# Kernel optimization log

Measured on AMD Instinct MI355X. Metric: run time of the kernel, lower is better.

The kernel has to match this reference:

```python
import jax, jax.numpy as jnp
import numpy as np

HID = 512
HEADS = 8
PF = 2048
EPS = 1e-5


def _layernorm(x, g, b):
    mu = jnp.mean(x, axis=-1, keepdims=True)
    var = jnp.var(x, axis=-1, keepdims=True)
    return (x - mu) * jax.lax.rsqrt(var + EPS) * g + b


def setup_inputs() -> dict:
    key = jax.random.key(0)
    ks = jax.random.split(key, 20)
    s = 0.02
    inp = {
        "trg": jax.random.normal(ks[0], (16, 1024, HID), jnp.float32),
        "src": jax.random.normal(ks[1], (16, 1024, HID), jnp.float32),
        "ln_g": jnp.ones((HID,), jnp.float32),
        "ln_b": jnp.zeros((HID,), jnp.float32),
        "wq": jax.random.normal(ks[2], (HID, HID), jnp.float32) * s,
        "bq": jnp.zeros((HID,), jnp.float32),
        "wk": jax.random.normal(ks[3], (HID, HID), jnp.float32) * s,
        "bk": jnp.zeros((HID,), jnp.float32),
        "wv": jax.random.normal(ks[4], (HID, HID), jnp.float32) * s,
        "bv": jnp.zeros((HID,), jnp.float32),
        "wo": jax.random.normal(ks[5], (HID, HID), jnp.float32) * s,
        "bo": jnp.zeros((HID,), jnp.float32),
        "pf1_w": jax.random.normal(ks[6], (PF, HID), jnp.float32) * s,
        "pf1_b": jnp.zeros((PF,), jnp.float32),
        "pf2_w": jax.random.normal(ks[7], (HID, PF), jnp.float32) * s,
        "pf2_b": jnp.zeros((HID,), jnp.float32),
        "fc1_w": jax.random.normal(ks[8], (256, HID), jnp.float32) * s,
        "fc1_b": jnp.zeros((256,), jnp.float32),
        "fc2_w": jax.random.normal(ks[9], (2, 256), jnp.float32) * s,
        "fc2_b": jnp.zeros((2,), jnp.float32),
    }
    return inp


def reference(trg, src, ln_g, ln_b, wq, bq, wk, bk, wv, bv, wo, bo,
              pf1_w, pf1_b, pf2_w, pf2_b, fc1_w, fc1_b, fc2_w, fc2_b):
    B, T, D = trg.shape
    S = src.shape[1]
    dh = D // HEADS

    # --- multi-head attention (Q=trg, K=V=src, no mask; dropout=eval/no-op) ---
    q = (trg @ wq.T + bq).reshape(B, T, HEADS, dh)
    k = (src @ wk.T + bk).reshape(B, S, HEADS, dh)
    v = (src @ wv.T + bv).reshape(B, S, HEADS, dh)
    scores = jnp.einsum('bqhd,bkhd->bhqk', q, k) / jnp.sqrt(jnp.float32(dh))
    attn = jax.nn.softmax(scores, axis=-1)
    ctx = jnp.einsum('bhqk,bkhd->bqhd', attn, v).reshape(B, T, D)
    sa_out = ctx @ wo.T + bo

    x = _layernorm(trg + sa_out, ln_g, ln_b)

    # --- position-wise feed-forward ---
    h = jax.nn.relu(x @ pf1_w.T + pf1_b)
    ff = h @ pf2_w.T + pf2_b
    x = _layernorm(x + ff, ln_g, ln_b)

    # --- norm-weighted sum pooling over sequence (vectorized) ---
    norm = jnp.linalg.norm(x, axis=2)              # [B, T]
    w = jax.nn.softmax(norm, axis=1)               # [B, T]
    pooled = jnp.einsum('bt,btd->bd', w, x)        # [B, D]

    label = jax.nn.relu(pooled @ fc1_w.T + fc1_b) @ fc2_w.T + fc2_b
    return label
```

## Files before the change

kernel.cpp:

```cpp
#include <hip/hip_runtime.h>

typedef __bf16 bf16x8 __attribute__((ext_vector_type(8)));
typedef float f32x4 __attribute__((ext_vector_type(4)));
typedef unsigned short u16;

__device__ __forceinline__ u16 f2bf(float f){
  unsigned u = __builtin_bit_cast(unsigned, f);
  u += 0x7fffu + ((u>>16)&1u);
  return (u16)(u>>16);
}
__device__ __forceinline__ float bf2f(u16 h){
  unsigned u = ((unsigned)h)<<16; return __builtin_bit_cast(float,u);
}
__device__ __forceinline__ bf16x8 ld8(const u16* p){ return *(const bf16x8*)p; }
__device__ __forceinline__ f32x4 mfma16(bf16x8 a, bf16x8 b, f32x4 c){
  return __builtin_amdgcn_mfma_f32_16x16x32_bf16(a,b,c,0,0,0);
}
__device__ __forceinline__ void gl16(const u16* g, u16* l){
  __builtin_amdgcn_global_load_lds(
    (const __attribute__((address_space(1))) unsigned int*)g,
    (__attribute__((address_space(3))) unsigned int*)l, 16, 0, 0);
}
__device__ __forceinline__ unsigned cvtpk(float a, float b){
  unsigned r;
  asm("v_cvt_pk_bf16_f32 %0, %1, %2" : "=v"(r) : "v"(a), "v"(b));
  return r;
}

#define QSC 0.18033688f

__global__ __launch_bounds__(256) void k_split2(const float* __restrict__ a,
    const float* __restrict__ b, u16* __restrict__ da, u16* __restrict__ db, int n){
  const float* s = blockIdx.y ? b : a;
  u16* d = blockIdx.y ? db : da;
  int i = (blockIdx.x*256 + threadIdx.x)*4;
  const int stride = gridDim.x*256*4;
  for(; i<n; i+=stride){
    float4 v = *(const float4*)(s+i);
    ushort4 H = {f2bf(v.x),f2bf(v.y),f2bf(v.z),f2bf(v.w)};
    *(ushort4*)(d+i)=H;
  }
}

struct SplitW { const float* s[6]; u16* d[6]; int n[6]; };
__global__ __launch_bounds__(256) void k_splitw(SplitW P){
  const int y = blockIdx.y;
  const float* s = P.s[y]; u16* d = P.d[y]; const int n = P.n[y];
  int i = (blockIdx.x*256 + threadIdx.x)*4;
  const int stride = gridDim.x*256*4;
  for(; i<n; i+=stride){
    float4 v = *(const float4*)(s+i);
    ushort4 H = {f2bf(v.x),f2bf(v.y),f2bf(v.z),f2bf(v.w)};
    *(ushort4*)(d+i)=H;
  }
}

template<int EPI>
__global__ __launch_bounds__(256) void k_gemm(
  const u16* __restrict__ A, const u16* __restrict__ W,
  const float* __restrict__ bias, int M, int N, int K,
  float* __restrict__ Cf, u16* __restrict__ Oh)
{
  __shared__ __align__(16) u16 sA[2][128*32], sW[2][128*32];
  const int tid = threadIdx.x, w = tid>>6, l = tid&63;
  const int l15 = l&15, g = l>>4;
  const int gx = gridDim.x;
  const int bid = blockIdx.y*gx + blockIdx.x;
  const int nwg = gx*gridDim.y;
  const int wgid = (bid&7)*(nwg>>3) + (bid>>3);
  const int m0 = (wgid/gx)*128, n0 = (wgid%gx)*128;
  const int wr = (w>>1)*64, wc = (w&1)*64;
  f32x4 acc[4][4] = {};
  const int sr = l>>2, sslot = l&3;
  const int scol = 8*((sslot - (sr>>1)) & 3);
  int offA[4], offW[4];
  #pragma unroll
  for(int i=0;i<4;i++){ const int R = wr+i*16+l15; offA[i] = R*32 + ((g+(R>>1))&3)*8; }
  #pragma unroll
  for(int j=0;j<4;j++){ const int C = wc+j*16+l15; offW[j] = C*32 + ((g+(C>>1))&3)*8; }
  const u16* Ab = A + (long)m0*K + scol;
  const u16* Wb = W + (long)n0*K + scol;
  const int nk = K>>5;

#define G_STAGE(BUF, T) { \
    const int k0 = (T)<<5; \
    _Pragma("unroll") \
    for(int i=0;i<2;i++){ \
      const int rows = i*64 + w*16; \
      gl16(Ab + (long)(rows+sr)*K + k0, sA[BUF] + rows*32); \
      gl16(Wb + (long)(rows+sr)*K + k0, sW[BUF] + rows*32); \
    } }

#define G_STEP(CUR, T) { \
    if((T)+1 < nk) G_STAGE(CUR^1, (T)+1); \
    bf16x8 av[4], wv[4]; \
    _Pragma("unroll") for(int i=0;i<4;i++) av[i] = *(const bf16x8*)(sA[CUR]+offA[i]); \
    _Pragma("unroll") for(int j=0;j<4;j++) wv[j] = *(const bf16x8*)(sW[CUR]+offW[j]); \
    _Pragma("unroll") for(int j=0;j<4;j++){ \
      _Pragma("unroll") for(int i=0;i<4;i++) acc[i][j] = mfma16(av[i], wv[j], acc[i][j]); } \
    __syncthreads(); }

  G_STAGE(0,0); __syncthreads();
  for(int t=0;t<nk;t+=2){ G_STEP(0,t); G_STEP(1,t+1); }
#undef G_STAGE
#undef G_STEP

  #pragma unroll
  for(int i=0;i<4;i++){
    #pragma unroll
    for(int j=0;j<4;j++){
      const int col  = n0 + wc + j*16 + l15;
      const float bb = bias ? bias[col] : 0.f;
      const int rowb = m0 + wr + i*16 + g*4;
      #pragma unroll
      for(int jj=0;jj<4;jj++){
        float v = acc[i][j][jj] + bb;
        const int row = rowb + jj;
        if constexpr(EPI==0){ Cf[(long)row*N + col] = v; }
        else { Oh[(long)row*N + col] = f2bf(fmaxf(v,0.f)); }
      }
    }
  }
}

__global__ __launch_bounds__(256) void k_qkv(
  const u16* __restrict__ trg_hi, const u16* __restrict__ src_hi,
  const u16* __restrict__ Wh,
  const float* __restrict__ bq, const float* __restrict__ bk, const float* __restrict__ bv,
  u16* __restrict__ Qb, u16* __restrict__ Kb, u16* __restrict__ Vt)
{
  __shared__ __align__(16) u16 sA[2][128*32], sW[2][128*32];
  const int tid = threadIdx.x, w = tid>>6, l = tid&63;
  const int l15 = l&15, g = l>>4;
  const int bid = blockIdx.x;
  const int wgid = (bid&7)*192 + (bid>>3);
  const int m0 = (wgid/12)*128, n0 = (wgid%12)*128;
  const u16* A = (n0<512)? trg_hi : src_hi;
  const float* bp = (n0<512)? bq : (n0<1024? bk : bv);
  const int nb = (n0<512)? 0 : (n0<1024? 512 : 1024);
  const int wr = (w>>1)*64, wc = (w&1)*64;
  f32x4 acc[4][4] = {};
  const int sr = l>>2, sslot = l&3;
  const int scol = 8*((sslot - (sr>>1)) & 3);
  int offA[4], offW[4];
  #pragma unroll
  for(int i=0;i<4;i++){ const int R = wr+i*16+l15; offA[i] = R*32 + ((g+(R>>1))&3)*8; }
  #pragma unroll
  for(int j=0;j<4;j++){ const int C = wc+j*16+l15; offW[j] = C*32 + ((g+(C>>1))&3)*8; }
  const u16* Ab = A  + (long)m0*512 + scol;
  const u16* Wb = Wh + (long)n0*512 + scol;

#define Q_STAGE(BUF, T) { \
    const int k0 = (T)<<5; \
    _Pragma("unroll") \
    for(int i=0;i<2;i++){ \
      const int rows = i*64 + w*16; \
      gl16(Ab + (long)(rows+sr)*512 + k0, sA[BUF] + rows*32); \
      gl16(Wb + (long)(rows+sr)*512 + k0, sW[BUF] + rows*32); \
    } }

#define Q_STEP(CUR, T) { \
    if((T)+1 < 16) Q_STAGE(CUR^1, (T)+1); \
    bf16x8 av[4], wv[4]; \
    _Pragma("unroll") for(int i=0;i<4;i++) av[i] = *(const bf16x8*)(sA[CUR]+offA[i]); \
    _Pragma("unroll") for(int j=0;j<4;j++) wv[j] = *(const bf16x8*)(sW[CUR]+offW[j]); \
    _Pragma("unroll") for(int j=0;j<4;j++){ \
      _Pragma("unroll") for(int i=0;i<4;i++) acc[i][j] = mfma16(av[i], wv[j], acc[i][j]); } \
    __syncthreads(); }

  Q_STAGE(0,0); __syncthreads();
  for(int t=0;t<16;t+=2){ Q_STEP(0,t); Q_STEP(1,t+1); }
#undef Q_STAGE
#undef Q_STEP

  #pragma unroll
  for(int i=0;i<4;i++){
    #pragma unroll
    for(int j=0;j<4;j++){
      const int col = n0 + wc + j*16 + l15;
      const int cl  = col - nb;
      const float bb = bp[cl];
      const int rowb = m0 + wr + i*16 + g*4;
      #pragma unroll
      for(int jj=0;jj<4;jj++){
        float v = acc[i][j][jj] + bb;
        const int row = rowb + jj;
        if(n0 < 512){ Qb[(long)row*512 + cl] = f2bf(v*QSC); }
        else if(n0 < 1024){ Kb[(long)row*512 + cl] = f2bf(v); }
        else {
          const int h = cl>>6, d = cl&63;
          const long dst = (((long)(row>>10)*8 + h)*64 + d)*1024
                         + ((row>>6)&15)*64 + (row&15)*4 + ((row>>4)&3);
          Vt[dst] = f2bf(v);
        }
      }
    }
  }
}

__global__ __launch_bounds__(512) void k_attn(
  const u16* __restrict__ Q, const u16* __restrict__ K,
  const u16* __restrict__ Vt, u16* __restrict__ O)
{
  __shared__ __align__(16) u16 sK[64*64], sV[64*64];
  __shared__ __align__(16) u16 Ph[8][16*72];
  const int bid = blockIdx.x;
  const int wg = (bid&7)*128 + (bid>>3);
  const int q0 = (wg&7)*128, hd = (wg>>3)&7, b = wg>>6;
  const int tid = threadIdx.x, w = tid>>6, l = tid&63, l15 = l&15, g = l>>4;
  const int qrow = q0 + w*16 + l15;
  const long qoff = (long)(b*1024 + qrow)*512 + hd*64 + g*8;
  bf16x8 qf[2] = { ld8(Q+qoff), ld8(Q+qoff+32) };
  const int srw = l>>3, sslot = l&7;
  const int scol = 8*(sslot ^ srw);
  const int rows = w*8;
  const u16* Kb = K + (long)b*1024*512 + hd*64;
  const u16* Vb = Vt + (long)(b*8+hd)*64*1024;
  f32x4 rs = {};
  f32x4 ctx[4] = {};
  for(int s0=0;s0<1024;s0+=64){
    gl16(Kb + (long)(s0+rows+srw)*512 + scol, sK + rows*64);
    gl16(Vb + (long)(rows+srw)*1024 + s0 + scol, sV + rows*64);
    __syncthreads();
    f32x4 sv[4];
    #pragma unroll
    for(int sf=0;sf<4;sf++){
      const int row = sf*16 + l15;
      f32x4 a = {};
      #pragma unroll
      for(int h=0;h<2;h++){
        const int ch = (g + 4*h) ^ (row&7);
        a = mfma16(qf[h], *(const bf16x8*)(sK + row*64 + ch*8), a);
      }
      sv[sf] = a;
    }
    float p[4][4];
    #pragma unroll
    for(int sf=0;sf<4;sf++){
      #pragma unroll
      for(int j=0;j<4;j++){
        p[sf][j] = exp2f(sv[sf][j]);
        rs[j] += p[sf][j];
      }
    }
    #pragma unroll
    for(int j=0;j<4;j++){
      uint2 pk = { cvtpk(p[0][j], p[1][j]), cvtpk(p[2][j], p[3][j]) };
      *(uint2*)(&Ph[w][(g*4+j)*72 + l15*4]) = pk;
    }
    #pragma unroll
    for(int ss=0;ss<2;ss++){
      bf16x8 pa = *(const bf16x8*)(&Ph[w][l15*72 + ss*32 + g*8]);
      #pragma unroll
      for(int df=0;df<4;df++){
        const int row = df*16 + l15;
        const int ch = (ss*4 + g) ^ (row&7);
        ctx[df] = mfma16(pa, *(const bf16x8*)(sV + row*64 + ch*8), ctx[df]);
      }
    }
    __syncthreads();
  }
  float inv[4];
  #pragma unroll
  for(int j=0;j<4;j++){
    float t = rs[j];
    #pragma unroll
    for(int mask=1;mask<16;mask<<=1) t += __shfl_xor(t, mask);
    inv[j] = 1.f/t;
  }
  #pragma unroll
  for(int df=0;df<4;df++){
    #pragma unroll
    for(int j=0;j<4;j++){
      const float v = ctx[df][j] * inv[j];
      const long off = (long)(b*1024 + q0 + w*16 + g*4 + j)*512 + hd*64 + df*16 + l15;
      O[off] = f2bf(v);
    }
  }
}

__global__ __launch_bounds__(256) void k_ln(
  const float* __restrict__ xa, const float* __restrict__ xb,
  const float* __restrict__ gg, const float* __restrict__ bvec,
  float* __restrict__ yf, u16* __restrict__ yh,
  float* __restrict__ norms)
{
  const int w = threadIdx.x>>6, l = threadIdx.x&63;
  const long rrow = (long)blockIdx.x*4 + w;
  const long base = rrow*512 + l*8;
  float4 a0 = *(const float4*)(xa+base), a1 = *(const float4*)(xa+base+4);
  float4 b0 = *(const float4*)(xb+base), b1 = *(const float4*)(xb+base+4);
  float v[8] = {a0.x+b0.x, a0.y+b0.y, a0.z+b0.z, a0.w+b0.w,
                a1.x+b1.x, a1.y+b1.y, a1.z+b1.z, a1.w+b1.w};
  float s=0.f, q=0.f;
  #pragma unroll
  for(int j=0;j<8;j++){ s += v[j]; q += v[j]*v[j]; }
  #pragma unroll
  for(int mask=1;mask<64;mask<<=1){ s += __shfl_xor(s,mask); q += __shfl_xor(q,mask); }
  const float mu  = s*(1.f/512.f);
  const float var = q*(1.f/512.f) - mu*mu;
  const float rstd = rsqrtf(var + 1e-5f);
  float y[8]; float nq = 0.f;
  #pragma unroll
  for(int j=0;j<8;j++){
    const int c = l*8+j;
    y[j] = (v[j]-mu)*rstd*gg[c] + bvec[c];
    nq += y[j]*y[j];
  }
  float4 t0={y[0],y[1],y[2],y[3]}, t1={y[4],y[5],y[6],y[7]};
  *(float4*)(yf+base)=t0; *(float4*)(yf+base+4)=t1;
  if(yh){
    u16 hv[8];
    #pragma unroll
    for(int j=0;j<8;j++){ hv[j]=f2bf(y[j]); }
    ushort4 hh0={hv[0],hv[1],hv[2],hv[3]}, hh1={hv[4],hv[5],hv[6],hv[7]};
    *(ushort4*)(yh+base)=hh0; *(ushort4*)(yh+base+4)=hh1;
  }
  if(norms){
    #pragma unroll
    for(int mask=1;mask<64;mask<<=1) nq += __shfl_xor(nq,mask);
    if(l==0) norms[rrow] = sqrtf(nq);
  }
}

__global__ __launch_bounds__(256) void k_pool2(const float* __restrict__ x2,
   const float* __restrict__ norms, float* __restrict__ partial)
{
  const int b = blockIdx.y, tc = blockIdx.z;
  const int col = blockIdx.x*256 + threadIdx.x;
  __shared__ float wsm[1024];
  __shared__ float red[4];
  const int tid = threadIdx.x, w = tid>>6, l = tid&63;
  float lm = -1e30f;
  for(int i=tid;i<1024;i+=256){ const float n = norms[b*1024+i]; wsm[i]=n; lm=fmaxf(lm,n); }
  #pragma unroll
  for(int mask=1;mask<64;mask<<=1) lm = fmaxf(lm, __shfl_xor(lm,mask));
  __syncthreads();
  if(l==0) red[w]=lm;
  __syncthreads();
  const float bm = fmaxf(fmaxf(red[0],red[1]), fmaxf(red[2],red[3]));
  __syncthreads();
  float ls = 0.f;
  for(int i=tid;i<1024;i+=256){ const float e = __expf(wsm[i]-bm); wsm[i]=e; ls+=e; }
  #pragma unroll
  for(int mask=1;mask<64;mask<<=1) ls += __shfl_xor(ls,mask);
  __syncthreads();
  if(l==0) red[w]=ls;
  __syncthreads();
  const float inv = 1.f/(red[0]+red[1]+red[2]+red[3]);
  float acc = 0.f;
  const int t0 = tc*128;
  for(int t=t0;t<t0+128;t++) acc += wsm[t]*x2[((long)b*1024+t)*512 + col];
  partial[((long)tc*16 + b)*512 + col] = acc*inv;
}

__global__ __launch_bounds__(256) void k_poolr(const float* __restrict__ partial,
   float* __restrict__ pooled)
{
  const int i = blockIdx.x*256 + threadIdx.x;
  float a = 0.f;
  #pragma unroll
  for(int tc=0;tc<8;tc++) a += partial[tc*8192 + i];
  pooled[i] = a;
}

__global__ __launch_bounds__(256) void k_head(const float* __restrict__ pooled,
  const float* __restrict__ w1, const float* __restrict__ b1,
  const float* __restrict__ w2, const float* __restrict__ b2,
  float* __restrict__ out)
{
  __shared__ float ps[16*512];
  __shared__ float h1[16*256];
  const int tid = threadIdx.x;
  for(int i=tid;i<16*512;i+=256) ps[i]=pooled[i];
  __syncthreads();
  float acc[16] = {};
  for(int k=0;k<512;k++){
    const float wv = w1[tid*512+k];
    #pragma unroll
    for(int i=0;i<16;i++) acc[i] += ps[i*512+k]*wv;
  }
  #pragma unroll
  for(int i=0;i<16;i++) h1[i*256+tid] = fmaxf(acc[i]+b1[tid], 0.f);
  __syncthreads();
  if(tid<32){
    const int i = tid>>1, o = tid&1;
    float a = b2[o];
    for(int k=0;k<256;k++) a += h1[i*256+k]*w2[o*256+k];
    out[i*2+o] = a;
  }
}

extern "C" void kernel_launch(void* const* d_in, const int* in_sizes, int n_in,
                              void* d_out, int out_size, void* d_ws, size_t ws_size,
                              hipStream_t stream)
{
  const float* trg  = (const float*)d_in[0];
  const float* src  = (const float*)d_in[1];
  const float* ln_g = (const float*)d_in[2];
  const float* ln_b = (const float*)d_in[3];
  const float* wq   = (const float*)d_in[4];  const float* bq  = (const float*)d_in[5];
  const float* wk   = (const float*)d_in[6];  const float* bk  = (const float*)d_in[7];
  const float* wv   = (const float*)d_in[8];  const float* bv  = (const float*)d_in[9];
  const float* wo   = (const float*)d_in[10]; const float* bo  = (const float*)d_in[11];
  const float* pf1w = (const float*)d_in[12]; const float* pf1b= (const float*)d_in[13];
  const float* pf2w = (const float*)d_in[14]; const float* pf2b= (const float*)d_in[15];
  const float* fc1w = (const float*)d_in[16]; const float* fc1b= (const float*)d_in[17];
  const float* fc2w = (const float*)d_in[18]; const float* fc2b= (const float*)d_in[19];
  float* out = (float*)d_out;

  char* ws = (char*)d_ws;
  const size_t PL = (size_t)16384*512*2;
  auto P = [&](int i)->u16*{ return (u16*)(ws + (size_t)i*PL); };
  u16 *src_hi=P(0), *trg_hi=P(1);
  u16 *Qb=P(2), *Kb=P(3), *Vt=P(4), *ctx=P(5);
  float* sa  = (float*)(ws + 0*PL);
  float* x1f = (float*)(ws + 2*PL);
  u16 *x1_hi = P(4);
  u16 *h_hi  = P(5);
  float* ffb = (float*)(ws + 0*PL);
  float* x2  = (float*)(ws + 5*PL);
  size_t off = 9*PL;
  auto carve = [&](size_t n)->char*{ char* p = ws+off; off += n; return p; };
  u16* wqkv_hi=(u16*)carve((size_t)1536*512*2);
  u16* wo_hi=(u16*)carve(512*512*2);
  u16* p1_hi=(u16*)carve((size_t)2048*512*2);
  u16* p2_hi=(u16*)carve((size_t)512*2048*2);
  float* norms  = (float*)carve(16384*4);
  float* partial= (float*)carve(8*16*512*4);
  float* pooled = (float*)carve(16*512*4);
  (void)ws_size; (void)in_sizes; (void)n_in; (void)out_size;

  const int NTOK = 16384;

  k_split2<<<dim3(8192,2),256,0,stream>>>(trg, src, trg_hi, src_hi, NTOK*512);
  SplitW sw;
  sw.s[0]=wq;  sw.d[0]=wqkv_hi;           sw.n[0]=512*512;
  sw.s[1]=wk;  sw.d[1]=wqkv_hi+512*512;   sw.n[1]=512*512;
  sw.s[2]=wv;  sw.d[2]=wqkv_hi+1024*512;  sw.n[2]=512*512;
  sw.s[3]=wo;  sw.d[3]=wo_hi;             sw.n[3]=512*512;
  sw.s[4]=pf1w; sw.d[4]=p1_hi;            sw.n[4]=2048*512;
  sw.s[5]=pf2w; sw.d[5]=p2_hi;            sw.n[5]=512*2048;
  k_splitw<<<dim3(512,6),256,0,stream>>>(sw);

  k_qkv<<<dim3(1536),256,0,stream>>>(trg_hi,src_hi,wqkv_hi,bq,bk,bv,Qb,Kb,Vt);

  k_attn<<<dim3(1024),512,0,stream>>>(Qb,Kb,Vt,ctx);

  k_gemm<0><<<dim3(4,128),256,0,stream>>>(ctx,wo_hi,bo,NTOK,512,512,sa,nullptr);
  k_ln<<<dim3(4096),256,0,stream>>>(trg, sa, ln_g, ln_b, x1f, x1_hi, nullptr);

  k_gemm<2><<<dim3(16,128),256,0,stream>>>(x1_hi,p1_hi,pf1b,NTOK,2048,512,nullptr,h_hi);
  k_gemm<0><<<dim3(4,128),256,0,stream>>>(h_hi,p2_hi,pf2b,NTOK,512,2048,ffb,nullptr);
  k_ln<<<dim3(4096),256,0,stream>>>(x1f, ffb, ln_g, ln_b, x2, nullptr, norms);

  k_pool2<<<dim3(2,16,8),256,0,stream>>>(x2, norms, partial);
  k_poolr<<<dim3(32),256,0,stream>>>(partial, pooled);
  k_head<<<1,256,0,stream>>>(pooled, fc1w, fc1b, fc2w, fc2b, out);
}
```

Measured before the change: 340.3 us.

## Fuse input bf16 conversion into QKV GEMM and store intermediates as bf16

Removes the separate fp32-to-bf16 conversion kernel for trg/src by loading fp32 activations in the QKV GEMM, converting in registers, and writing to LDS. Out-projection and FFN2 outputs, LayerNorm outputs, and the pooled input are now stored in bf16 instead of fp32. This cuts global memory traffic and one launch. The cost is register-staged A loads in place of async LDS loads, and reduced precision in the residual path.

```diff
diff --git a/kernel.cpp b/kernel.cpp
--- a/kernel.cpp
+++ b/kernel.cpp
@@ -28,19 +28,6 @@
 }
 
 #define QSC 0.18033688f
-
-__global__ __launch_bounds__(256) void k_split2(const float* __restrict__ a,
-    const float* __restrict__ b, u16* __restrict__ da, u16* __restrict__ db, int n){
-  const float* s = blockIdx.y ? b : a;
-  u16* d = blockIdx.y ? db : da;
-  int i = (blockIdx.x*256 + threadIdx.x)*4;
-  const int stride = gridDim.x*256*4;
-  for(; i<n; i+=stride){
-    float4 v = *(const float4*)(s+i);
-    ushort4 H = {f2bf(v.x),f2bf(v.y),f2bf(v.z),f2bf(v.w)};
-    *(ushort4*)(d+i)=H;
-  }
-}
 
 struct SplitW { const float* s[6]; u16* d[6]; int n[6]; };
 __global__ __launch_bounds__(256) void k_splitw(SplitW P){
@@ -117,6 +104,7 @@
         float v = acc[i][j][jj] + bb;
         const int row = rowb + jj;
         if constexpr(EPI==0){ Cf[(long)row*N + col] = v; }
+        else if constexpr(EPI==1){ Oh[(long)row*N + col] = f2bf(v); }
         else { Oh[(long)row*N + col] = f2bf(fmaxf(v,0.f)); }
       }
     }
@@ -124,7 +112,7 @@
 }
 
 __global__ __launch_bounds__(256) void k_qkv(
-  const u16* __restrict__ trg_hi, const u16* __restrict__ src_hi,
+  const float* __restrict__ trg, const float* __restrict__ src,
   const u16* __restrict__ Wh,
   const float* __restrict__ bq, const float* __restrict__ bk, const float* __restrict__ bv,
   u16* __restrict__ Qb, u16* __restrict__ Kb, u16* __restrict__ Vt)
@@ -135,42 +123,65 @@
   const int bid = blockIdx.x;
   const int wgid = (bid&7)*192 + (bid>>3);
   const int m0 = (wgid/12)*128, n0 = (wgid%12)*128;
-  const u16* A = (n0<512)? trg_hi : src_hi;
+  const float* A = (n0<512)? trg : src;
   const float* bp = (n0<512)? bq : (n0<1024? bk : bv);
   const int nb = (n0<512)? 0 : (n0<1024? 512 : 1024);
   const int wr = (w>>1)*64, wc = (w&1)*64;
   f32x4 acc[4][4] = {};
   const int sr = l>>2, sslot = l&3;
   const int scol = 8*((sslot - (sr>>1)) & 3);
+  const int arow = tid>>1;
+  const int ahalf = (tid&1)*16;
+  const int c0 = (tid&1)*2;
+  const int awo0 = arow*32 + ((c0   + (arow>>1))&3)*8;
+  const int awo1 = arow*32 + ((c0+1 + (arow>>1))&3)*8;
   int offA[4], offW[4];
   #pragma unroll
   for(int i=0;i<4;i++){ const int R = wr+i*16+l15; offA[i] = R*32 + ((g+(R>>1))&3)*8; }
   #pragma unroll
   for(int j=0;j<4;j++){ const int C = wc+j*16+l15; offW[j] = C*32 + ((g+(C>>1))&3)*8; }
-  const u16* Ab = A  + (long)m0*512 + scol;
-  const u16* Wb = Wh + (long)n0*512 + scol;
-
-#define Q_STAGE(BUF, T) { \
+  const float* Ab = A  + (long)(m0+arow)*512 + ahalf;
+  const u16*   Wb = Wh + (long)n0*512 + scol;
+
+#define QA_LOAD(T) { const int k0=(T)<<5; \
+    a0_ = *(const float4*)(Ab + k0); \
+    a1_ = *(const float4*)(Ab + k0 + 4); \
+    a2_ = *(const float4*)(Ab + k0 + 8); \
+    a3_ = *(const float4*)(Ab + k0 + 12); }
+
+#define QA_WRITE(BUF) { \
+    uint4 u0 = { cvtpk(a0_.x,a0_.y), cvtpk(a0_.z,a0_.w), cvtpk(a1_.x,a1_.y), cvtpk(a1_.z,a1_.w) }; \
+    uint4 u1 = { cvtpk(a2_.x,a2_.y), cvtpk(a2_.z,a2_.w), cvtpk(a3_.x,a3_.y), cvtpk(a3_.z,a3_.w) }; \
+    *(uint4*)(sA[BUF] + awo0) = u0; \
+    *(uint4*)(sA[BUF] + awo1) = u1; }
+
+#define QW_STAGE(BUF, T) { \
     const int k0 = (T)<<5; \
     _Pragma("unroll") \
     for(int i=0;i<2;i++){ \
       const int rows = i*64 + w*16; \
-      gl16(Ab + (long)(rows+sr)*512 + k0, sA[BUF] + rows*32); \
       gl16(Wb + (long)(rows+sr)*512 + k0, sW[BUF] + rows*32); \
     } }
 
 #define Q_STEP(CUR, T) { \
-    if((T)+1 < 16) Q_STAGE(CUR^1, (T)+1); \
+    float4 a0_,a1_,a2_,a3_; \
+    const bool pf = (T)+1 < 16; \
+    if(pf){ QA_LOAD((T)+1); QW_STAGE(CUR^1,(T)+1); } \
     bf16x8 av[4], wv[4]; \
     _Pragma("unroll") for(int i=0;i<4;i++) av[i] = *(const bf16x8*)(sA[CUR]+offA[i]); \
     _Pragma("unroll") for(int j=0;j<4;j++) wv[j] = *(const bf16x8*)(sW[CUR]+offW[j]); \
     _Pragma("unroll") for(int j=0;j<4;j++){ \
       _Pragma("unroll") for(int i=0;i<4;i++) acc[i][j] = mfma16(av[i], wv[j], acc[i][j]); } \
+    if(pf){ QA_WRITE(CUR^1); } \
     __syncthreads(); }
 
-  Q_STAGE(0,0); __syncthreads();
+  { float4 a0_,a1_,a2_,a3_;
+    QA_LOAD(0); QW_STAGE(0,0); QA_WRITE(0); }
+  __syncthreads();
   for(int t=0;t<16;t+=2){ Q_STEP(0,t); Q_STEP(1,t+1); }
-#undef Q_STAGE
+#undef QA_LOAD
+#undef QA_WRITE
+#undef QW_STAGE
 #undef Q_STEP
 
   #pragma unroll
@@ -279,19 +290,29 @@
   }
 }
 
+template<int XAF>
 __global__ __launch_bounds__(256) void k_ln(
-  const float* __restrict__ xa, const float* __restrict__ xb,
+  const float* __restrict__ xaf, const u16* __restrict__ xab,
+  const u16* __restrict__ xbb,
   const float* __restrict__ gg, const float* __restrict__ bvec,
-  float* __restrict__ yf, u16* __restrict__ yh,
-  float* __restrict__ norms)
+  u16* __restrict__ yh, float* __restrict__ norms)
 {
   const int w = threadIdx.x>>6, l = threadIdx.x&63;
   const long rrow = (long)blockIdx.x*4 + w;
   const long base = rrow*512 + l*8;
-  float4 a0 = *(const float4*)(xa+base), a1 = *(const float4*)(xa+base+4);
-  float4 b0 = *(const float4*)(xb+base), b1 = *(const float4*)(xb+base+4);
-  float v[8] = {a0.x+b0.x, a0.y+b0.y, a0.z+b0.z, a0.w+b0.w,
-                a1.x+b1.x, a1.y+b1.y, a1.z+b1.z, a1.w+b1.w};
+  float va[8];
+  if constexpr(XAF){
+    float4 a0 = *(const float4*)(xaf+base), a1 = *(const float4*)(xaf+base+4);
+    va[0]=a0.x; va[1]=a0.y; va[2]=a0.z; va[3]=a0.w;
+    va[4]=a1.x; va[5]=a1.y; va[6]=a1.z; va[7]=a1.w;
+  } else {
+    ushort4 a0 = *(const ushort4*)(xab+base), a1 = *(const ushort4*)(xab+base+4);
+    va[0]=bf2f(a0.x); va[1]=bf2f(a0.y); va[2]=bf2f(a0.z); va[3]=bf2f(a0.w);
+    va[4]=bf2f(a1.x); va[5]=bf2f(a1.y); va[6]=bf2f(a1.z); va[7]=bf2f(a1.w);
+  }
+  ushort4 b0 = *(const ushort4*)(xbb+base), b1 = *(const ushort4*)(xbb+base+4);
+  float v[8] = {va[0]+bf2f(b0.x), va[1]+bf2f(b0.y), va[2]+bf2f(b0.z), va[3]+bf2f(b0.w),
+                va[4]+bf2f(b1.x), va[5]+bf2f(b1.y), va[6]+bf2f(b1.z), va[7]+bf2f(b1.w)};
   float s=0.f, q=0.f;
   #pragma unroll
   for(int j=0;j<8;j++){ s += v[j]; q += v[j]*v[j]; }
@@ -307,15 +328,11 @@
     y[j] = (v[j]-mu)*rstd*gg[c] + bvec[c];
     nq += y[j]*y[j];
   }
-  float4 t0={y[0],y[1],y[2],y[3]}, t1={y[4],y[5],y[6],y[7]};
-  *(float4*)(yf+base)=t0; *(float4*)(yf+base+4)=t1;
-  if(yh){
-    u16 hv[8];
-    #pragma unroll
-    for(int j=0;j<8;j++){ hv[j]=f2bf(y[j]); }
-    ushort4 hh0={hv[0],hv[1],hv[2],hv[3]}, hh1={hv[4],hv[5],hv[6],hv[7]};
-    *(ushort4*)(yh+base)=hh0; *(ushort4*)(yh+base+4)=hh1;
-  }
+  u16 hv[8];
+  #pragma unroll
+  for(int j=0;j<8;j++){ hv[j]=f2bf(y[j]); }
+  ushort4 hh0={hv[0],hv[1],hv[2],hv[3]}, hh1={hv[4],hv[5],hv[6],hv[7]};
+  *(ushort4*)(yh+base)=hh0; *(ushort4*)(yh+base+4)=hh1;
   if(norms){
     #pragma unroll
     for(int mask=1;mask<64;mask<<=1) nq += __shfl_xor(nq,mask);
@@ -323,7 +340,7 @@
   }
 }
 
-__global__ __launch_bounds__(256) void k_pool2(const float* __restrict__ x2,
+__global__ __launch_bounds__(256) void k_pool2(const u16* __restrict__ x2,
    const float* __restrict__ norms, float* __restrict__ partial)
 {
   const int b = blockIdx.y, tc = blockIdx.z;
@@ -350,7 +367,7 @@
   const float inv = 1.f/(red[0]+red[1]+red[2]+red[3]);
   float acc = 0.f;
   const int t0 = tc*128;
-  for(int t=t0;t<t0+128;t++) acc += wsm[t]*x2[((long)b*1024+t)*512 + col];
+  for(int t=t0;t<t0+128;t++) acc += wsm[t]*bf2f(x2[((long)b*1024+t)*512 + col]);
   partial[((long)tc*16 + b)*512 + col] = acc*inv;
 }
 
@@ -412,15 +429,13 @@
   char* ws = (char*)d_ws;
   const size_t PL = (size_t)16384*512*2;
   auto P = [&](int i)->u16*{ return (u16*)(ws + (size_t)i*PL); };
-  u16 *src_hi=P(0), *trg_hi=P(1);
-  u16 *Qb=P(2), *Kb=P(3), *Vt=P(4), *ctx=P(5);
-  float* sa  = (float*)(ws + 0*PL);
-  float* x1f = (float*)(ws + 2*PL);
-  u16 *x1_hi = P(4);
-  u16 *h_hi  = P(5);
-  float* ffb = (float*)(ws + 0*PL);
-  float* x2  = (float*)(ws + 5*PL);
-  size_t off = 9*PL;
+  u16 *Qb=P(0), *Kb=P(1), *Vt=P(2), *ctx=P(3);
+  u16 *sa_bf = P(4);
+  u16 *x1_hi = P(5);
+  u16 *h_hi  = P(0);
+  u16 *ffb_bf= P(4);
+  u16 *x2_bf = P(6);
+  size_t off = 7*PL;
   auto carve = [&](size_t n)->char*{ char* p = ws+off; off += n; return p; };
   u16* wqkv_hi=(u16*)carve((size_t)1536*512*2);
   u16* wo_hi=(u16*)carve(512*512*2);
@@ -433,7 +448,6 @@
 
   const int NTOK = 16384;
 
-  k_split2<<<dim3(8192,2),256,0,stream>>>(trg, src, trg_hi, src_hi, NTOK*512);
   SplitW sw;
   sw.s[0]=wq;  sw.d[0]=wqkv_hi;           sw.n[0]=512*512;
   sw.s[1]=wk;  sw.d[1]=wqkv_hi+512*512;   sw.n[1]=512*512;
@@ -443,18 +457,18 @@
   sw.s[5]=pf2w; sw.d[5]=p2_hi;            sw.n[5]=512*2048;
   k_splitw<<<dim3(512,6),256,0,stream>>>(sw);
 
-  k_qkv<<<dim3(1536),256,0,stream>>>(trg_hi,src_hi,wqkv_hi,bq,bk,bv,Qb,Kb,Vt);
+  k_qkv<<<dim3(1536),256,0,stream>>>(trg,src,wqkv_hi,bq,bk,bv,Qb,Kb,Vt);
 
   k_attn<<<dim3(1024),512,0,stream>>>(Qb,Kb,Vt,ctx);
 
-  k_gemm<0><<<dim3(4,128),256,0,stream>>>(ctx,wo_hi,bo,NTOK,512,512,sa,nullptr);
-  k_ln<<<dim3(4096),256,0,stream>>>(trg, sa, ln_g, ln_b, x1f, x1_hi, nullptr);
+  k_gemm<1><<<dim3(4,128),256,0,stream>>>(ctx,wo_hi,bo,NTOK,512,512,nullptr,sa_bf);
+  k_ln<1><<<dim3(4096),256,0,stream>>>(trg, nullptr, sa_bf, ln_g, ln_b, x1_hi, nullptr);
 
   k_gemm<2><<<dim3(16,128),256,0,stream>>>(x1_hi,p1_hi,pf1b,NTOK,2048,512,nullptr,h_hi);
-  k_gemm<0><<<dim3(4,128),256,0,stream>>>(h_hi,p2_hi,pf2b,NTOK,512,2048,ffb,nullptr);
-  k_ln<<<dim3(4096),256,0,stream>>>(x1f, ffb, ln_g, ln_b, x2, nullptr, norms);
-
-  k_pool2<<<dim3(2,16,8),256,0,stream>>>(x2, norms, partial);
+  k_gemm<1><<<dim3(4,128),256,0,stream>>>(h_hi,p2_hi,pf2b,NTOK,512,2048,nullptr,ffb_bf);
+  k_ln<0><<<dim3(4096),256,0,stream>>>(nullptr, x1_hi, ffb_bf, ln_g, ln_b, x2_bf, norms);
+
+  k_pool2<<<dim3(2,16,8),256,0,stream>>>(x2_bf, norms, partial);
   k_poolr<<<dim3(32),256,0,stream>>>(partial, pooled);
   k_head<<<1,256,0,stream>>>(pooled, fc1w, fc1b, fc2w, fc2b, out);
 }
```

New measurement: 325.4 us. 4.4% less time.
